# Performance work log

Measured on AMD Instinct MI355X. Metric: run time of the kernel, lower is better.

The kernel has to match this reference:

```python
import jax, jax.numpy as jnp
import numpy as np


def setup_inputs() -> dict:
    key = jax.random.key(0)
    ks = jax.random.split(key, 7)
    n, d_in, d_h = 1024, 1024, 512
    scale = 1.0 / np.sqrt(d_in)
    return {
        "vectors": jax.random.normal(ks[0], (n, d_in), dtype=jnp.float32),
        "W_h": jax.random.normal(ks[1], (d_h, d_in), dtype=jnp.float32) * scale,
        "b_h": jax.random.normal(ks[2], (d_h,), dtype=jnp.float32) * 0.01,
        "W_m": jax.random.normal(ks[3], (d_h, d_in), dtype=jnp.float32) * scale,
        "b_m": jax.random.normal(ks[4], (d_h,), dtype=jnp.float32) * 0.01,
        "w2": jax.random.normal(ks[5], (d_h,), dtype=jnp.float32) * (1.0 / np.sqrt(d_h)),
        "b2": jax.random.normal(ks[6], (1,), dtype=jnp.float32) * 0.01,
    }


def reference(vectors, W_h, b_h, W_m, b_m, w2, b2):
    # Two linear projections: [n, d_h]
    h = vectors @ W_h.T + b_h  # head representations
    m = vectors @ W_m.T + b_m  # modifier representations
    # Pairwise broadcast add: pair[i, j, :] = h[i] + m[j]  -> [n, n, d_h]
    pair = jnp.tanh(h[:, None, :] + m[None, :, :])
    # Linear to scalar + squeeze -> [n, n]
    scores = jnp.einsum("ijh,h->ij", pair, w2) + b2[0]
    return scores
```

## Files before the change

kernel.cpp:

```cpp
#include <hip/hip_runtime.h>
#include <hip/hip_bf16.h>

#define D_IN  1024
#define D_H   512
#define L2E2  2.885390081777927f
#define ECLAMP 15.0f

typedef _Float16 half8 __attribute__((ext_vector_type(8)));
typedef _Float16 half4v __attribute__((ext_vector_type(4)));
typedef float f32x4 __attribute__((ext_vector_type(4)));

__global__ __launch_bounds__(256) void cvt_kernel(
    const float* __restrict__ V,
    const float* __restrict__ Wh, const float* __restrict__ Wm,
    _Float16* __restrict__ Vh, _Float16* __restrict__ Wf)
{
  const int idx = blockIdx.x * 256 + threadIdx.x;
  {
    float4 x = ((const float4*)V)[idx];
    half4v o = { (_Float16)x.x, (_Float16)x.y, (_Float16)x.z, (_Float16)x.w };
    ((half4v*)Vh)[idx] = o;
  }
  {
    const float4* p = (idx < 131072) ? ((const float4*)Wh + idx)
                                     : ((const float4*)Wm + (idx - 131072));
    float4 x = *p;
    half4v o = { (_Float16)x.x, (_Float16)x.y, (_Float16)x.z, (_Float16)x.w };
    ((half4v*)Wf)[idx] = o;
  }
}

__global__ __launch_bounds__(512, 2) void proj_mfma_kernel(
    const _Float16* __restrict__ Vh, const _Float16* __restrict__ Wf,
    const float* __restrict__ bh, const float* __restrict__ bm,
    float* __restrict__ C)
{
  const int tid  = threadIdx.x;
  const int lane = tid & 63;
  const int wid  = tid >> 6;
  const int wi   = wid >> 2, wj = wid & 3;
  const int bid  = blockIdx.x;
  const int swz  = (bid & 7) * 32 + (bid >> 3);
  const int i0   = (swz & 15) * 64;
  const int j0   = (swz >> 4) * 64;
  const int r16  = lane & 15;
  const int kg   = lane >> 4;

  const _Float16* A0 = Vh + (size_t)(i0 + 32*wi + r16) * 1024 + kg*8;
  const _Float16* A1 = A0 + 16 * 1024;
  const _Float16* B0 = Wf + (size_t)(j0 + 16*wj + r16) * 1024 + kg*8;

  f32x4 acc0 = {0.f,0.f,0.f,0.f}, acc1 = acc0;
  #pragma unroll 8
  for (int k0 = 0; k0 < D_IN; k0 += 32) {
    half8 a0 = *(const half8*)(A0 + k0);
    half8 a1 = *(const half8*)(A1 + k0);
    half8 b0 = *(const half8*)(B0 + k0);
    acc0 = __builtin_amdgcn_mfma_f32_16x16x32_f16(a0, b0, acc0, 0, 0, 0);
    acc1 = __builtin_amdgcn_mfma_f32_16x16x32_f16(a1, b0, acc1, 0, 0, 0);
  }

  const float* biasp = (j0 < D_H) ? (bh + j0) : (bm + (j0 - D_H));
  const int jl = 16*wj + r16;
  const float bias = biasp[jl];
  #pragma unroll
  for (int fi = 0; fi < 2; ++fi) {
    const f32x4 acc = fi ? acc1 : acc0;
    #pragma unroll
    for (int rr = 0; rr < 4; ++rr) {
      const int il = 32*wi + 16*fi + 4*kg + rr;
      float x = (acc[rr] + bias) * L2E2;
      x = fminf(fmaxf(x, -ECLAMP), ECLAMP);
      C[(size_t)(i0 + il) * 1024 + j0 + jl] = __builtin_amdgcn_exp2f(x);
    }
  }
}

__global__ __launch_bounds__(256) void proj_kernel(
    const float* __restrict__ V,
    const float* __restrict__ Wh, const float* __restrict__ bh,
    const float* __restrict__ Wm, const float* __restrict__ bm,
    float* __restrict__ C)
{
  __shared__ float As[16][68];
  __shared__ float Bs[16][68];

  const int tid = threadIdx.x;
  const int i0  = (blockIdx.x & 15) * 64, j0 = (blockIdx.x >> 4) * 64;
  const int ti  = tid >> 4, tj = tid & 15;
  const int sr  = tid >> 2;
  const int sk  = (tid & 3) << 2;

  const float* Wbase = (j0 < D_H) ? (Wh + (size_t)j0 * D_IN)
                                  : (Wm + (size_t)(j0 - D_H) * D_IN);
  const float* biasp = (j0 < D_H) ? (bh + j0) : (bm + (j0 - D_H));

  const float* arow = V     + (size_t)(i0 + sr) * D_IN + sk;
  const float* brow = Wbase + (size_t)sr        * D_IN + sk;

  float acc[4][4] = {};
  for (int k0 = 0; k0 < D_IN; k0 += 16) {
    float4 av = *(const float4*)(arow + k0);
    float4 bv = *(const float4*)(brow + k0);
    As[sk+0][sr] = av.x; As[sk+1][sr] = av.y; As[sk+2][sr] = av.z; As[sk+3][sr] = av.w;
    Bs[sk+0][sr] = bv.x; Bs[sk+1][sr] = bv.y; Bs[sk+2][sr] = bv.z; Bs[sk+3][sr] = bv.w;
    __syncthreads();
    #pragma unroll
    for (int kk = 0; kk < 16; ++kk) {
      float4 a = *(const float4*)&As[kk][4*ti];
      float4 b = *(const float4*)&Bs[kk][4*tj];
      #pragma unroll
      for (int x = 0; x < 4; ++x)
        #pragma unroll
        for (int y = 0; y < 4; ++y)
          acc[x][y] = fmaf((&a.x)[x], (&b.x)[y], acc[x][y]);
    }
    __syncthreads();
  }

  const int jl = 4 * tj;
  #pragma unroll
  for (int aa = 0; aa < 4; ++aa) {
    const int i = i0 + 4*ti + aa;
    float4 o;
    #pragma unroll
    for (int bb = 0; bb < 4; ++bb) {
      float x = (acc[aa][bb] + biasp[jl+bb]) * L2E2;
      x = fminf(fmaxf(x, -ECLAMP), ECLAMP);
      (&o.x)[bb] = __builtin_amdgcn_exp2f(x);
    }
    *(float4*)(C + (size_t)i * 1024 + j0 + jl) = o;
  }
}

__global__ __launch_bounds__(256, 4) void score_kernel(
    const float* __restrict__ C,
    const float* __restrict__ w2,
    const float* __restrict__ b2,
    float* __restrict__ out)
{
  __shared__ float hs[2][32][34];
  __shared__ float ms[2][32][34];
  __shared__ float wred[4];

  const int tid = threadIdx.x;
  const int bi  = blockIdx.x & 31;
  const int bj  = blockIdx.x >> 5;
  const int i0  = bi * 32, j0 = bj * 32;
  const int ti  = tid >> 4, tj = tid & 15;

  const int sr  = tid >> 3;
  const int sk  = (tid & 7) << 2;

  float sw = 0.f;
  for (int t = tid; t < D_H; t += 256) sw += w2[t];
  #pragma unroll
  for (int off = 32; off > 0; off >>= 1) sw += __shfl_down(sw, off, 64);
  if ((tid & 63) == 0) wred[tid >> 6] = sw;

  const float* hrow = C + (size_t)(i0 + sr) * 1024 + sk;
  const float* mrow = C + (size_t)(j0 + sr) * 1024 + D_H + sk;

  float4 hv = *(const float4*)(hrow);
  float4 mv = *(const float4*)(mrow);

  float acc[2][2] = {};
  int p = 0;

  for (int k0 = 0; k0 < D_H; k0 += 32) {
    *(float2*)&hs[p][sr][sk]     = make_float2(hv.x, hv.y);
    *(float2*)&hs[p][sr][sk + 2] = make_float2(hv.z, hv.w);
    *(float2*)&ms[p][sr][sk]     = make_float2(mv.x, mv.y);
    *(float2*)&ms[p][sr][sk + 2] = make_float2(mv.z, mv.w);
    __syncthreads();

    if (k0 + 32 < D_H) {
      hv = *(const float4*)(hrow + k0 + 32);
      mv = *(const float4*)(mrow + k0 + 32);
    }

    #pragma unroll
    for (int g = 0; g < 8; ++g) {
      const int kk = 4 * g;
      const float wA = w2[k0 + kk + 0];
      const float wB = w2[k0 + kk + 1];
      const float wC = w2[k0 + kk + 2];
      const float wD = w2[k0 + kk + 3];
      float2 em_[2][2], eh_[2][2];
      #pragma unroll
      for (int c = 0; c < 2; ++c) {
        em_[c][0] = *(const float2*)&ms[p][tj + 16*c][kk];
        em_[c][1] = *(const float2*)&ms[p][tj + 16*c][kk + 2];
      }
      #pragma unroll
      for (int a = 0; a < 2; ++a) {
        eh_[a][0] = *(const float2*)&hs[p][ti + 16*a][kk];
        eh_[a][1] = *(const float2*)&hs[p][ti + 16*a][kk + 2];
      }
      #pragma unroll
      for (int a = 0; a < 2; ++a)
        #pragma unroll
        for (int c = 0; c < 2; ++c) {
          float uA = fmaf(eh_[a][0].x, em_[c][0].x, 1.f);
          float uB = fmaf(eh_[a][0].y, em_[c][0].y, 1.f);
          float uC = fmaf(eh_[a][1].x, em_[c][1].x, 1.f);
          float uD = fmaf(eh_[a][1].y, em_[c][1].y, 1.f);
          float dAB = uA * uB, dCD = uC * uD;
          float nAB = fmaf(wB, uA, wA * uB);
          float nCD = fmaf(wD, uC, wC * uD);
          float den = dAB * dCD;
          float num = fmaf(nCD, dAB, nAB * dCD);
          acc[a][c] = fmaf(num, __builtin_amdgcn_rcpf(den), acc[a][c]);
        }
    }
    p ^= 1;
  }

  const float base = b2[0] + wred[0] + wred[1] + wred[2] + wred[3];
  #pragma unroll
  for (int a = 0; a < 2; ++a) {
    const int i = i0 + ti + 16*a;
    #pragma unroll
    for (int c = 0; c < 2; ++c) {
      const int j = j0 + tj + 16*c;
      out[(size_t)i * 1024 + j] = fmaf(-2.f, acc[a][c], base);
    }
  }
}

extern "C" void kernel_launch(void* const* d_in, const int* in_sizes, int n_in,
                              void* d_out, int out_size, void* d_ws, size_t ws_size,
                              hipStream_t stream) {
  const float* V  = (const float*)d_in[0];
  const float* Wh = (const float*)d_in[1];
  const float* bh = (const float*)d_in[2];
  const float* Wm = (const float*)d_in[3];
  const float* bm = (const float*)d_in[4];
  const float* w2 = (const float*)d_in[5];
  const float* b2 = (const float*)d_in[6];
  float* outp = (float*)d_out;

  char* ws = (char*)d_ws;
  float* C = (float*)ws;

  if (ws_size >= (size_t)(8u << 20)) {
    _Float16* Vh = (_Float16*)(ws + (4u << 20));
    _Float16* Wf = (_Float16*)(ws + (6u << 20));
    cvt_kernel<<<dim3(1024), dim3(256), 0, stream>>>(V, Wh, Wm, Vh, Wf);
    proj_mfma_kernel<<<dim3(256), dim3(512), 0, stream>>>(Vh, Wf, bh, bm, C);
  } else {
    proj_kernel<<<dim3(256), dim3(256), 0, stream>>>(V, Wh, bh, Wm, bm, C);
  }
  score_kernel<<<dim3(1024), dim3(256), 0, stream>>>(C, w2, b2, outp);
}
```

Baseline: 89.06 us.

## Split-K projection GEMM with LDS reduction and enlarge score tile to 64x32

The projection MFMA kernel now uses 32x32 output tiles over 1024 blocks. Each of the four waves handles a quarter of K, and the partial sums are reduced through shared memory before a vectorised bias, exp2 and store epilogue. This aims for better CU occupancy and coalesced float4 writes. The score kernel doubles its row tile to 64, so each m tile loaded from shared memory is reused across four h rows instead of two, and the grid halves to 512 blocks. The cost is higher register and LDS pressure (launch bounds drop to 2 blocks per SM) and fewer blocks for the dominant score kernel.

```diff
diff --git a/kernel.cpp b/kernel.cpp
--- a/kernel.cpp
+++ b/kernel.cpp
@@ -30,50 +30,69 @@
   }
 }
 
-__global__ __launch_bounds__(512, 2) void proj_mfma_kernel(
+__global__ __launch_bounds__(256, 4) void proj_mfma_kernel(
     const _Float16* __restrict__ Vh, const _Float16* __restrict__ Wf,
     const float* __restrict__ bh, const float* __restrict__ bm,
     float* __restrict__ C)
 {
+  __shared__ float red[4][32][34];
+
   const int tid  = threadIdx.x;
   const int lane = tid & 63;
   const int wid  = tid >> 6;
-  const int wi   = wid >> 2, wj = wid & 3;
   const int bid  = blockIdx.x;
-  const int swz  = (bid & 7) * 32 + (bid >> 3);
-  const int i0   = (swz & 15) * 64;
-  const int j0   = (swz >> 4) * 64;
+  const int swz  = (bid & 7) * 128 + (bid >> 3);
+  const int i0   = (swz & 31) * 32;
+  const int j0   = (swz >> 5) * 32;
   const int r16  = lane & 15;
   const int kg   = lane >> 4;
-
-  const _Float16* A0 = Vh + (size_t)(i0 + 32*wi + r16) * 1024 + kg*8;
+  const int kb   = wid * 256;
+
+  const _Float16* A0 = Vh + (size_t)(i0 + r16) * 1024 + kb + kg*8;
   const _Float16* A1 = A0 + 16 * 1024;
-  const _Float16* B0 = Wf + (size_t)(j0 + 16*wj + r16) * 1024 + kg*8;
-
-  f32x4 acc0 = {0.f,0.f,0.f,0.f}, acc1 = acc0;
-  #pragma unroll 8
-  for (int k0 = 0; k0 < D_IN; k0 += 32) {
+  const _Float16* B0 = Wf + (size_t)(j0 + r16) * 1024 + kb + kg*8;
+  const _Float16* B1 = B0 + 16 * 1024;
+
+  f32x4 acc00 = {0.f,0.f,0.f,0.f}, acc01 = acc00, acc10 = acc00, acc11 = acc00;
+  #pragma unroll 4
+  for (int k0 = 0; k0 < 256; k0 += 32) {
     half8 a0 = *(const half8*)(A0 + k0);
     half8 a1 = *(const half8*)(A1 + k0);
     half8 b0 = *(const half8*)(B0 + k0);
-    acc0 = __builtin_amdgcn_mfma_f32_16x16x32_f16(a0, b0, acc0, 0, 0, 0);
-    acc1 = __builtin_amdgcn_mfma_f32_16x16x32_f16(a1, b0, acc1, 0, 0, 0);
-  }
-
+    half8 b1 = *(const half8*)(B1 + k0);
+    acc00 = __builtin_amdgcn_mfma_f32_16x16x32_f16(a0, b0, acc00, 0, 0, 0);
+    acc01 = __builtin_amdgcn_mfma_f32_16x16x32_f16(a0, b1, acc01, 0, 0, 0);
+    acc10 = __builtin_amdgcn_mfma_f32_16x16x32_f16(a1, b0, acc10, 0, 0, 0);
+    acc11 = __builtin_amdgcn_mfma_f32_16x16x32_f16(a1, b1, acc11, 0, 0, 0);
+  }
+
+  #pragma unroll
+  for (int fi = 0; fi < 2; ++fi) {
+    #pragma unroll
+    for (int fj = 0; fj < 2; ++fj) {
+      const f32x4 acc = (fi == 0) ? (fj == 0 ? acc00 : acc01)
+                                  : (fj == 0 ? acc10 : acc11);
+      #pragma unroll
+      for (int rr = 0; rr < 4; ++rr)
+        red[wid][16*fi + 4*kg + rr][16*fj + r16] = acc[rr];
+    }
+  }
+  __syncthreads();
+
+  const int row = tid >> 3;
+  const int c4  = (tid & 7) * 4;
   const float* biasp = (j0 < D_H) ? (bh + j0) : (bm + (j0 - D_H));
-  const int jl = 16*wj + r16;
-  const float bias = biasp[jl];
-  #pragma unroll
-  for (int fi = 0; fi < 2; ++fi) {
-    const f32x4 acc = fi ? acc1 : acc0;
-    #pragma unroll
-    for (int rr = 0; rr < 4; ++rr) {
-      const int il = 32*wi + 16*fi + 4*kg + rr;
-      float x = (acc[rr] + bias) * L2E2;
-      x = fminf(fmaxf(x, -ECLAMP), ECLAMP);
-      C[(size_t)(i0 + il) * 1024 + j0 + jl] = __builtin_amdgcn_exp2f(x);
-    }
-  }
+  float4 bias = *(const float4*)(biasp + c4);
+  float4 o;
+  #pragma unroll
+  for (int q = 0; q < 4; ++q) {
+    float s = red[0][row][c4+q] + red[1][row][c4+q]
+            + red[2][row][c4+q] + red[3][row][c4+q];
+    float x = (s + (&bias.x)[q]) * L2E2;
+    x = fminf(fmaxf(x, -ECLAMP), ECLAMP);
+    (&o.x)[q] = __builtin_amdgcn_exp2f(x);
+  }
+  *(float4*)(C + (size_t)(i0 + row) * 1024 + j0 + c4) = o;
 }
 
 __global__ __launch_bounds__(256) void proj_kernel(
@@ -133,20 +152,20 @@
   }
 }
 
-__global__ __launch_bounds__(256, 4) void score_kernel(
+__global__ __launch_bounds__(256, 2) void score_kernel(
     const float* __restrict__ C,
     const float* __restrict__ w2,
     const float* __restrict__ b2,
     float* __restrict__ out)
 {
-  __shared__ float hs[2][32][34];
+  __shared__ float hs[2][64][34];
   __shared__ float ms[2][32][34];
   __shared__ float wred[4];
 
   const int tid = threadIdx.x;
-  const int bi  = blockIdx.x & 31;
-  const int bj  = blockIdx.x >> 5;
-  const int i0  = bi * 32, j0 = bj * 32;
+  const int bi  = blockIdx.x & 15;
+  const int bj  = blockIdx.x >> 4;
+  const int i0  = bi * 64, j0 = bj * 32;
   const int ti  = tid >> 4, tj = tid & 15;
 
   const int sr  = tid >> 3;
@@ -158,25 +177,30 @@
   for (int off = 32; off > 0; off >>= 1) sw += __shfl_down(sw, off, 64);
   if ((tid & 63) == 0) wred[tid >> 6] = sw;
 
-  const float* hrow = C + (size_t)(i0 + sr) * 1024 + sk;
-  const float* mrow = C + (size_t)(j0 + sr) * 1024 + D_H + sk;
-
-  float4 hv = *(const float4*)(hrow);
-  float4 mv = *(const float4*)(mrow);
-
-  float acc[2][2] = {};
+  const float* hrow0 = C + (size_t)(i0 + sr)      * 1024 + sk;
+  const float* hrow1 = C + (size_t)(i0 + sr + 32) * 1024 + sk;
+  const float* mrow  = C + (size_t)(j0 + sr) * 1024 + D_H + sk;
+
+  float4 hv0 = *(const float4*)(hrow0);
+  float4 hv1 = *(const float4*)(hrow1);
+  float4 mv  = *(const float4*)(mrow);
+
+  float acc[4][2] = {};
   int p = 0;
 
   for (int k0 = 0; k0 < D_H; k0 += 32) {
-    *(float2*)&hs[p][sr][sk]     = make_float2(hv.x, hv.y);
-    *(float2*)&hs[p][sr][sk + 2] = make_float2(hv.z, hv.w);
-    *(float2*)&ms[p][sr][sk]     = make_float2(mv.x, mv.y);
-    *(float2*)&ms[p][sr][sk + 2] = make_float2(mv.z, mv.w);
+    *(float2*)&hs[p][sr][sk]          = make_float2(hv0.x, hv0.y);
+    *(float2*)&hs[p][sr][sk + 2]      = make_float2(hv0.z, hv0.w);
+    *(float2*)&hs[p][sr + 32][sk]     = make_float2(hv1.x, hv1.y);
+    *(float2*)&hs[p][sr + 32][sk + 2] = make_float2(hv1.z, hv1.w);
+    *(float2*)&ms[p][sr][sk]          = make_float2(mv.x, mv.y);
+    *(float2*)&ms[p][sr][sk + 2]      = make_float2(mv.z, mv.w);
     __syncthreads();
 
     if (k0 + 32 < D_H) {
-      hv = *(const float4*)(hrow + k0 + 32);
-      mv = *(const float4*)(mrow + k0 + 32);
+      hv0 = *(const float4*)(hrow0 + k0 + 32);
+      hv1 = *(const float4*)(hrow1 + k0 + 32);
+      mv  = *(const float4*)(mrow  + k0 + 32);
     }
 
     #pragma unroll
@@ -186,19 +210,19 @@
       const float wB = w2[k0 + kk + 1];
       const float wC = w2[k0 + kk + 2];
       const float wD = w2[k0 + kk + 3];
-      float2 em_[2][2], eh_[2][2];
+      float2 em_[2][2], eh_[4][2];
       #pragma unroll
       for (int c = 0; c < 2; ++c) {
         em_[c][0] = *(const float2*)&ms[p][tj + 16*c][kk];
         em_[c][1] = *(const float2*)&ms[p][tj + 16*c][kk + 2];
       }
       #pragma unroll
-      for (int a = 0; a < 2; ++a) {
+      for (int a = 0; a < 4; ++a) {
         eh_[a][0] = *(const float2*)&hs[p][ti + 16*a][kk];
         eh_[a][1] = *(const float2*)&hs[p][ti + 16*a][kk + 2];
       }
       #pragma unroll
-      for (int a = 0; a < 2; ++a)
+      for (int a = 0; a < 4; ++a)
         #pragma unroll
         for (int c = 0; c < 2; ++c) {
           float uA = fmaf(eh_[a][0].x, em_[c][0].x, 1.f);
@@ -218,7 +242,7 @@
 
   const float base = b2[0] + wred[0] + wred[1] + wred[2] + wred[3];
   #pragma unroll
-  for (int a = 0; a < 2; ++a) {
+  for (int a = 0; a < 4; ++a) {
     const int i = i0 + ti + 16*a;
     #pragma unroll
     for (int c = 0; c < 2; ++c) {
@@ -247,9 +271,9 @@
     _Float16* Vh = (_Float16*)(ws + (4u << 20));
     _Float16* Wf = (_Float16*)(ws + (6u << 20));
     cvt_kernel<<<dim3(1024), dim3(256), 0, stream>>>(V, Wh, Wm, Vh, Wf);
-    proj_mfma_kernel<<<dim3(256), dim3(512), 0, stream>>>(Vh, Wf, bh, bm, C);
+    proj_mfma_kernel<<<dim3(1024), dim3(256), 0, stream>>>(Vh, Wf, bh, bm, C);
   } else {
     proj_kernel<<<dim3(256), dim3(256), 0, stream>>>(V, Wh, bh, Wm, bm, C);
   }
-  score_kernel<<<dim3(1024), dim3(256), 0, stream>>>(C, w2, b2, outp);
-}
+  score_kernel<<<dim3(512), dim3(256), 0, stream>>>(C, w2, b2, outp);
+}
```

New measurement: 80.94 us. 9.1% less time.
